# Optimization experiments

Measured on AMD Instinct MI355X. Metric: run time of the kernel, lower is better.

Reference implementation:

```python
import jax, jax.numpy as jnp
import numpy as np

N_NODES = 100000
N_EDGES = 1600000
D_IN = 64
D_HID = 64


def setup_inputs() -> dict:
    key = jax.random.key(0)
    k1, k2, k3, k4, k5 = jax.random.split(key, 5)
    x = jax.random.normal(k1, (N_NODES, D_IN), dtype=jnp.float32)
    edge_index = jax.random.randint(k2, (2, N_EDGES), 0, N_NODES, dtype=jnp.int64)
    edge_weight = jax.random.uniform(k3, (N_EDGES,), dtype=jnp.float32)
    # GCNConv glorot-initialized linear weights (bias=False)
    s0 = (6.0 / (D_IN + D_HID)) ** 0.5
    W0 = jax.random.uniform(k4, (D_IN, D_HID), minval=-s0, maxval=s0, dtype=jnp.float32)
    s1 = (6.0 / (D_HID + D_HID)) ** 0.5
    W1 = jax.random.uniform(k5, (D_HID, D_HID), minval=-s1, maxval=s1, dtype=jnp.float32)
    return {"x": x, "edge_index": edge_index, "edge_weight": edge_weight, "W0": W0, "W1": W1}


def _gcn_layer(x, W, src, dst, edge_weight, deg_inv_sqrt, n_nodes):
    # h = X W  (bias=False)
    h = x @ W  # [N, D]
    # symmetric normalization including self-loops (weight 1)
    norm = deg_inv_sqrt[src] * edge_weight * deg_inv_sqrt[dst]  # [E]
    # gather src features, scale, scatter-sum at dst
    agg = jax.ops.segment_sum(norm[:, None] * h[src], dst, num_segments=n_nodes)
    # self-loop contribution: norm_ii = deg_inv_sqrt[i]^2 * 1
    agg = agg + (deg_inv_sqrt * deg_inv_sqrt)[:, None] * h
    return jax.nn.relu(agg)  # dropout is identity in eval mode


def reference(x, edge_index, edge_weight, W0, W1):
    src, dst = edge_index[0], edge_index[1]
    # degree with self-loops (self-loop weight = 1), aggregated at dst (source_to_target flow)
    deg = jax.ops.segment_sum(edge_weight, dst, num_segments=N_NODES) + 1.0
    deg_inv_sqrt = jax.lax.rsqrt(deg)
    x = _gcn_layer(x, W0, src, dst, edge_weight, deg_inv_sqrt, N_NODES)
    x = _gcn_layer(x, W1, src, dst, edge_weight, deg_inv_sqrt, N_NODES)
    return x
```

## Files before the change

### kernel.cpp

```cpp
#include <hip/hip_runtime.h>
#include <hip/hip_fp16.h>

#define D 64
#define BSH 9
#define BSZ (1 << BSH)
#define PB 4096
#define CAPR 10240
#define CAPU (2 * CAPR)
#define FASTU (BSZ * 32)
#define SCAP 9216

__global__ __launch_bounds__(256) void initcur(int* __restrict__ ccur, int nbuck) {
    int t = threadIdx.x;
    if (t < nbuck) ccur[t] = t * CAPR;
    if (t == 255) ccur[255] = 0;
}

__global__ __launch_bounds__(512) void bucket1(const int* __restrict__ src,
                                               const int* __restrict__ dst,
                                               const float* __restrict__ ew,
                                               int* __restrict__ ccur,
                                               int2* __restrict__ pairs2,
                                               int E, int nbuck) {
    __shared__ int hist[512];
    __shared__ int lbase[512];
    __shared__ int gbase[512];
    __shared__ int w0s[PB];
    __shared__ int w1s[PB];
    __shared__ unsigned char bids[PB];
    int t = threadIdx.x;
    hist[t] = 0;
    __syncthreads();
    int e0 = blockIdx.x * PB;
    int cnt = min(PB, E - e0);
    int b[8], lr[8], w0[8], w1[8];
    int i8 = t * 8;
    bool full8 = (i8 + 8 <= cnt);
    if (full8) {
        int4   sa = *(const int4*)&src[e0 + i8];
        int4   sb = *(const int4*)&src[e0 + i8 + 4];
        int4   da = *(const int4*)&dst[e0 + i8];
        int4   db = *(const int4*)&dst[e0 + i8 + 4];
        float4 wa = *(const float4*)&ew[e0 + i8];
        float4 wb = *(const float4*)&ew[e0 + i8 + 4];
        int ss[8] = {sa.x, sa.y, sa.z, sa.w, sb.x, sb.y, sb.z, sb.w};
        int ds[8] = {da.x, da.y, da.z, da.w, db.x, db.y, db.z, db.w};
        float wv[8] = {wa.x, wa.y, wa.z, wa.w, wb.x, wb.y, wb.z, wb.w};
#pragma unroll
        for (int k = 0; k < 8; ++k) {
            b[k]  = ds[k] >> BSH;
            w0[k] = ss[k] | ((ds[k] & (BSZ - 1)) << 17);
            w1[k] = __float_as_int(wv[k]);
            lr[k] = atomicAdd(&hist[b[k]], 1);
        }
    } else {
#pragma unroll
        for (int k = 0; k < 8; ++k) {
            int idx = i8 + k;
            if (idx < cnt) {
                int d = dst[e0 + idx];
                b[k]  = d >> BSH;
                w0[k] = src[e0 + idx] | ((d & (BSZ - 1)) << 17);
                w1[k] = __float_as_int(ew[e0 + idx]);
                lr[k] = atomicAdd(&hist[b[k]], 1);
            }
        }
    }
    __syncthreads();
    int hv = hist[t];
    lbase[t] = hv;
    __syncthreads();
    for (int off = 1; off < 512; off <<= 1) {
        int u = (t >= off) ? lbase[t - off] : 0;
        __syncthreads();
        lbase[t] += u;
        __syncthreads();
    }
    int excl = lbase[t] - hv;
    __syncthreads();
    lbase[t] = excl;
    if (t < nbuck && hv > 0) gbase[t] = atomicAdd(&ccur[t], hv);
    __syncthreads();
#pragma unroll
    for (int k = 0; k < 8; ++k) {
        int idx = i8 + k;
        if (idx < cnt) {
            int slot = lbase[b[k]] + lr[k];
            w0s[slot] = w0[k];
            w1s[slot] = w1[k];
            bids[slot] = (unsigned char)b[k];
        }
    }
    __syncthreads();
    for (int i = t; i < cnt; i += 512) {
        int bb = bids[i];
        int pos = gbase[bb] + (i - lbase[bb]);
        pairs2[pos] = make_int2(w0s[i], w1s[i]);
    }
}

__global__ __launch_bounds__(512) void sort2(int2* __restrict__ pairs2,
                                             unsigned int* __restrict__ fastU,
                                             const int* __restrict__ ccur,
                                             int2* __restrict__ extRng,
                                             unsigned int* __restrict__ extU,
                                             int* __restrict__ gext,
                                             float* __restrict__ dis,
                                             int N, int nbuck) {
    __shared__ int2 se[SCAP];
    __shared__ int cnt[512];
    __shared__ float sdeg[512];
    __shared__ int ebase[512];
    int b = blockIdx.x;
    int t = threadIdx.x;
    int baseR = b * CAPR;
    int baseU = b * CAPU;
    int cntb = min(ccur[b] - baseR, SCAP);
    for (int i = t; i < cntb; i += 512) se[i] = pairs2[baseR + i];
    cnt[t] = 0;
    sdeg[t] = 0.0f;
    __syncthreads();
    for (int i = t; i < cntb; i += 512) {
        int2 p = se[i];
        int dl = (p.x >> 17) & (BSZ - 1);
        int lr = atomicAdd(&cnt[dl], 1);
        atomicAdd(&sdeg[dl], __int_as_float(p.y));
        se[i].x = p.x | (lr << 26);
    }
    __syncthreads();
    int node = (b << BSH) + t;
    int cntv = cnt[t];
    int pc = (node < N) ? ((cntv + 1 + 31) & ~31) : 0;
    int extLen = (pc > 32) ? (pc - 32) : 0;
    int extBase = 0;
    if (extLen > 0) extBase = atomicAdd(gext, extLen);
    float dloc = rsqrtf(sdeg[t] + 1.0f);
    __syncthreads();
    sdeg[t]  = dloc;
    ebase[t] = extBase;
    if (node < N) {
        extRng[node] = make_int2(extBase, extBase + extLen);
        dis[node]    = dloc;
    }
    for (int i = t; i < FASTU; i += 512) fastU[baseU + i] = 0u;
    __syncthreads();
    for (int i = t; i < cntb; i += 512) {
        int2 p = se[i];
        int dl = (p.x >> 17) & (BSZ - 1);
        int s  = p.x & 0x1FFFF;
        int rank = ((unsigned int)p.x) >> 26;
        float w = __int_as_float(p.y) * sdeg[dl];
        unsigned int h = (unsigned int)__half_as_ushort(__float2half_rn(w));
        unsigned int packed = ((unsigned int)s << 15) | ((h + 1u) >> 1);
        if (rank < 32) fastU[baseU + dl * 32 + rank] = packed;
        else           extU[ebase[dl] + rank - 32]   = packed;
    }
    if (node < N) {
        unsigned int h = (unsigned int)__half_as_ushort(__float2half_rn(dloc));
        unsigned int selfp = ((unsigned int)node << 15) | ((h + 1u) >> 1);
        if (cntv < 32) fastU[baseU + t * 32 + cntv] = selfp;
        else           extU[extBase + cntv - 32]    = selfp;
        for (int i = cntv + 1 - 32; i < extLen; ++i) extU[extBase + i] = 0u;
    }
}

__global__ __launch_bounds__(256) void gemm64h(const float* __restrict__ X,
                                               const float* __restrict__ W,
                                               const float* __restrict__ dis,
                                               __half* __restrict__ Hb, int n) {
    __shared__ float Ws[64 * 64];
    __shared__ float Xs[16 * 64];
    for (int t = threadIdx.x; t < 64 * 64; t += 256) Ws[t] = W[t];
    int row0 = blockIdx.x * 16;
    for (int t = threadIdx.x; t < 16 * 64; t += 256) {
        int r = row0 + (t >> 6);
        Xs[t] = (r < n) ? X[r * 64 + (t & 63)] : 0.0f;
    }
    __syncthreads();
    int r  = threadIdx.x >> 4;
    int jc = (threadIdx.x & 15) * 4;
    float4 acc = make_float4(0.f, 0.f, 0.f, 0.f);
#pragma unroll
    for (int k = 0; k < 64; ++k) {
        float xv = Xs[r * 64 + k];
        float4 w = *(const float4*)&Ws[k * 64 + jc];
        acc.x += xv * w.x; acc.y += xv * w.y; acc.z += xv * w.z; acc.w += xv * w.w;
    }
    int rr = row0 + r;
    if (rr < n) {
        float ds = dis[rr];
        ushort4 pk;
        pk.x = __half_as_ushort(__float2half(ds * acc.x));
        pk.y = __half_as_ushort(__float2half(ds * acc.y));
        pk.z = __half_as_ushort(__float2half(ds * acc.z));
        pk.w = __half_as_ushort(__float2half(ds * acc.w));
        *(ushort4*)&Hb[rr * 64 + jc] = pk;
    }
}

__device__ __forceinline__ void acc_group(unsigned int pv, int g, int fl,
                                          const __half* __restrict__ Hb,
                                          __half2 a0[4], __half2 a1[4],
                                          __half2 a2[4], __half2 a3[4]) {
    unsigned int q0 = __shfl(pv, g, 64);
    unsigned int q1 = __shfl(pv, g + 8, 64);
    unsigned int q2 = __shfl(pv, g + 16, 64);
    unsigned int q3 = __shfl(pv, g + 24, 64);
    uint4 r0 = *(const uint4*)(Hb + (size_t)(q0 >> 15) * 64 + fl);
    uint4 r1 = *(const uint4*)(Hb + (size_t)(q1 >> 15) * 64 + fl);
    uint4 r2 = *(const uint4*)(Hb + (size_t)(q2 >> 15) * 64 + fl);
    uint4 r3 = *(const uint4*)(Hb + (size_t)(q3 >> 15) * 64 + fl);
    __half2 w0 = __half2half2(__ushort_as_half((unsigned short)((q0 & 0x7FFFu) << 1)));
    __half2 w1 = __half2half2(__ushort_as_half((unsigned short)((q1 & 0x7FFFu) << 1)));
    __half2 w2 = __half2half2(__ushort_as_half((unsigned short)((q2 & 0x7FFFu) << 1)));
    __half2 w3 = __half2half2(__ushort_as_half((unsigned short)((q3 & 0x7FFFu) << 1)));
    const __half2* h0 = (const __half2*)&r0;
    const __half2* h1 = (const __half2*)&r1;
    const __half2* h2 = (const __half2*)&r2;
    const __half2* h3 = (const __half2*)&r3;
#pragma unroll
    for (int k = 0; k < 4; ++k) {
        a0[k] = __hfma2(w0, h0[k], a0[k]);
        a1[k] = __hfma2(w1, h1[k], a1[k]);
        a2[k] = __hfma2(w2, h2[k], a2[k]);
        a3[k] = __hfma2(w3, h3[k], a3[k]);
    }
}

__global__ __launch_bounds__(256) void gather64(const unsigned int* __restrict__ fastU,
                                                const unsigned int* __restrict__ extU,
                                                const int2* __restrict__ extRng,
                                                const __half* __restrict__ Hb,
                                                float* __restrict__ OUT, int N) {
    int node = blockIdx.x * 4 + (threadIdx.x >> 6);
    if (node >= N) return;
    int lane = threadIdx.x & 63;
    int g    = lane >> 3;
    int fl   = (lane & 7) * 8;
    int l31  = lane & 31;
    int fbase = (node >> BSH) * CAPU + (node & (BSZ - 1)) * 32;
    unsigned int pv = fastU[fbase + l31];
    int2 er = extRng[node];
    __half2 z = __float2half2_rn(0.0f);
    __half2 a0[4] = {z, z, z, z};
    __half2 a1[4] = {z, z, z, z};
    __half2 a2[4] = {z, z, z, z};
    __half2 a3[4] = {z, z, z, z};
    acc_group(pv, g, fl, Hb, a0, a1, a2, a3);
    for (int e = er.x; e < er.y; e += 32)
        acc_group(extU[e + l31], g, fl, Hb, a0, a1, a2, a3);
    __half2 a[4];
#pragma unroll
    for (int k = 0; k < 4; ++k)
        a[k] = __hadd2(__hadd2(a0[k], a1[k]), __hadd2(a2[k], a3[k]));
#pragma unroll
    for (int m = 8; m < 64; m <<= 1) {
#pragma unroll
        for (int k = 0; k < 4; ++k) {
            unsigned u = __shfl_xor(*(unsigned*)&a[k], m, 64);
            a[k] = __hadd2(a[k], *(__half2*)&u);
        }
    }
    if (g < 2) {
        int o = g * 2;
        float2 f0 = __half22float2(a[o]);
        float2 f1 = __half22float2(a[o + 1]);
        float4 vv;
        vv.x = fmaxf(f0.x, 0.0f);
        vv.y = fmaxf(f0.y, 0.0f);
        vv.z = fmaxf(f1.x, 0.0f);
        vv.w = fmaxf(f1.y, 0.0f);
        *(float4*)&OUT[node * 64 + fl + g * 4] = vv;
    }
}

extern "C" void kernel_launch(void* const* d_in, const int* in_sizes, int n_in,
                              void* d_out, int out_size, void* d_ws, size_t ws_size,
                              hipStream_t stream) {
    const float* x  = (const float*)d_in[0];
    const int*   ei = (const int*)d_in[1];
    const float* ew = (const float*)d_in[2];
    const float* W0 = (const float*)d_in[3];
    const float* W1 = (const float*)d_in[4];
    float* out = (float*)d_out;

    const int N = in_sizes[0] / D;
    const int E = in_sizes[2];
    const int* src = ei;
    const int* dst = ei + E;

    const int nbuck = (N + BSZ - 1) >> BSH;
    const int Na = (N + 1 + 255) & ~255;

    float* dis     = (float*)d_ws;
    int2*  extRng  = (int2*)((int*)d_ws + Na);
    int*   ccur    = (int*)d_ws + 3 * Na;
    int2*  pairs2  = (int2*)((int*)d_ws + 3 * Na + 1024);
    unsigned int* fastU = (unsigned int*)pairs2;
    __half* Hb     = (__half*)((int*)d_ws + 3 * Na + 1024 + (size_t)nbuck * CAPU);
    unsigned int* extU = (unsigned int*)((__half*)Hb + (size_t)N * D);

    const int nb1 = (E + PB - 1) / PB;

    initcur<<<1, 256, 0, stream>>>(ccur, nbuck);
    bucket1<<<nb1, 512, 0, stream>>>(src, dst, ew, ccur, pairs2, E, nbuck);
    sort2<<<nbuck, 512, 0, stream>>>(pairs2, fastU, ccur, extRng, extU,
                                     ccur + 255, dis, N, nbuck);

    const int gemm_grid   = (N + 15) / 16;
    const int gather_grid = (N + 3) / 4;

    gemm64h<<<gemm_grid, 256, 0, stream>>>(x, W0, dis, Hb, N);
    gather64<<<gather_grid, 256, 0, stream>>>(fastU, extU, extRng, Hb, out, N);

    gemm64h<<<gemm_grid, 256, 0, stream>>>(out, W1, dis, Hb, N);
    gather64<<<gather_grid, 256, 0, stream>>>(fastU, extU, extRng, Hb, out, N);
}
```

Before: 190.9 us.

## Use wave-shuffle scan, half-size fast slots for small nodes, fp16 intermediate layer

Result: no change. 190.2 us (-0.3%).

```diff
diff --git a/kernel.cpp b/kernel.cpp
--- a/kernel.cpp
+++ b/kernel.cpp
@@ -25,6 +25,7 @@
     __shared__ int hist[512];
     __shared__ int lbase[512];
     __shared__ int gbase[512];
+    __shared__ int wsum[8];
     __shared__ int w0s[PB];
     __shared__ int w1s[PB];
     __shared__ unsigned char bids[PB];
@@ -68,16 +69,19 @@
     }
     __syncthreads();
     int hv = hist[t];
-    lbase[t] = hv;
-    __syncthreads();
-    for (int off = 1; off < 512; off <<= 1) {
-        int u = (t >= off) ? lbase[t - off] : 0;
-        __syncthreads();
-        lbase[t] += u;
-        __syncthreads();
-    }
-    int excl = lbase[t] - hv;
-    __syncthreads();
+    int lane = t & 63, wv8 = t >> 6;
+    int s = hv;
+#pragma unroll
+    for (int off = 1; off < 64; off <<= 1) {
+        int u = __shfl_up(s, off, 64);
+        if (lane >= off) s += u;
+    }
+    if (lane == 63) wsum[wv8] = s;
+    __syncthreads();
+    int woff = 0;
+#pragma unroll
+    for (int w = 0; w < 8; ++w) { int x = wsum[w]; if (w < wv8) woff += x; }
+    int excl = s + woff - hv;
     lbase[t] = excl;
     if (t < nbuck && hv > 0) gbase[t] = atomicAdd(&ccur[t], hv);
     __syncthreads();
@@ -130,16 +134,18 @@
     __syncthreads();
     int node = (b << BSH) + t;
     int cntv = cnt[t];
-    int pc = (node < N) ? ((cntv + 1 + 31) & ~31) : 0;
+    int tot  = cntv + 1;
+    int pc   = (tot <= 16) ? 16 : ((tot + 31) & ~31);
     int extLen = (pc > 32) ? (pc - 32) : 0;
     int extBase = 0;
-    if (extLen > 0) extBase = atomicAdd(gext, extLen);
+    if (node < N && extLen > 0) extBase = atomicAdd(gext, extLen);
     float dloc = rsqrtf(sdeg[t] + 1.0f);
     __syncthreads();
     sdeg[t]  = dloc;
     ebase[t] = extBase;
     if (node < N) {
-        extRng[node] = make_int2(extBase, extBase + extLen);
+        int flag = (pc == 16) ? (1 << 30) : 0;
+        extRng[node] = make_int2(extBase | flag, extBase + extLen);
         dis[node]    = dloc;
     }
     for (int i = t; i < FASTU; i += 512) fastU[baseU + i] = 0u;
@@ -164,7 +170,8 @@
     }
 }
 
-__global__ __launch_bounds__(256) void gemm64h(const float* __restrict__ X,
+template<int HIN>
+__global__ __launch_bounds__(256) void gemm64h(const void* __restrict__ Xv,
                                                const float* __restrict__ W,
                                                const float* __restrict__ dis,
                                                __half* __restrict__ Hb, int n) {
@@ -174,7 +181,12 @@
     int row0 = blockIdx.x * 16;
     for (int t = threadIdx.x; t < 16 * 64; t += 256) {
         int r = row0 + (t >> 6);
-        Xs[t] = (r < n) ? X[r * 64 + (t & 63)] : 0.0f;
+        float v = 0.0f;
+        if (r < n) {
+            if constexpr (HIN) v = __half2float(((const __half*)Xv)[r * 64 + (t & 63)]);
+            else               v = ((const float*)Xv)[r * 64 + (t & 63)];
+        }
+        Xs[t] = v;
     }
     __syncthreads();
     int r  = threadIdx.x >> 4;
@@ -227,11 +239,12 @@
     }
 }
 
+template<int HOUT>
 __global__ __launch_bounds__(256) void gather64(const unsigned int* __restrict__ fastU,
                                                 const unsigned int* __restrict__ extU,
                                                 const int2* __restrict__ extRng,
                                                 const __half* __restrict__ Hb,
-                                                float* __restrict__ OUT, int N) {
+                                                void* __restrict__ OUTv, int N) {
     int node = blockIdx.x * 4 + (threadIdx.x >> 6);
     if (node >= N) return;
     int lane = threadIdx.x & 63;
@@ -241,13 +254,47 @@
     int fbase = (node >> BSH) * CAPU + (node & (BSZ - 1)) * 32;
     unsigned int pv = fastU[fbase + l31];
     int2 er = extRng[node];
+    bool small = (er.x & (1 << 30)) != 0;
+    int eb = er.x & 0x3FFFFFFF;
     __half2 z = __float2half2_rn(0.0f);
     __half2 a0[4] = {z, z, z, z};
     __half2 a1[4] = {z, z, z, z};
     __half2 a2[4] = {z, z, z, z};
     __half2 a3[4] = {z, z, z, z};
-    acc_group(pv, g, fl, Hb, a0, a1, a2, a3);
-    for (int e = er.x; e < er.y; e += 32)
+    {
+        unsigned int q0 = __shfl(pv, g, 64);
+        unsigned int q1 = __shfl(pv, g + 8, 64);
+        unsigned int q2 = __shfl(pv, g + 16, 64);
+        unsigned int q3 = __shfl(pv, g + 24, 64);
+        uint4 r0 = *(const uint4*)(Hb + (size_t)(q0 >> 15) * 64 + fl);
+        uint4 r1 = *(const uint4*)(Hb + (size_t)(q1 >> 15) * 64 + fl);
+        uint4 r2, r3;
+        if (!small) {
+            r2 = *(const uint4*)(Hb + (size_t)(q2 >> 15) * 64 + fl);
+            r3 = *(const uint4*)(Hb + (size_t)(q3 >> 15) * 64 + fl);
+        }
+        __half2 w0 = __half2half2(__ushort_as_half((unsigned short)((q0 & 0x7FFFu) << 1)));
+        __half2 w1 = __half2half2(__ushort_as_half((unsigned short)((q1 & 0x7FFFu) << 1)));
+        const __half2* h0 = (const __half2*)&r0;
+        const __half2* h1 = (const __half2*)&r1;
+#pragma unroll
+        for (int k = 0; k < 4; ++k) {
+            a0[k] = __hfma2(w0, h0[k], a0[k]);
+            a1[k] = __hfma2(w1, h1[k], a1[k]);
+        }
+        if (!small) {
+            __half2 w2 = __half2half2(__ushort_as_half((unsigned short)((q2 & 0x7FFFu) << 1)));
+            __half2 w3 = __half2half2(__ushort_as_half((unsigned short)((q3 & 0x7FFFu) << 1)));
+            const __half2* h2 = (const __half2*)&r2;
+            const __half2* h3 = (const __half2*)&r3;
+#pragma unroll
+            for (int k = 0; k < 4; ++k) {
+                a2[k] = __hfma2(w2, h2[k], a2[k]);
+                a3[k] = __hfma2(w3, h3[k], a3[k]);
+            }
+        }
+    }
+    for (int e = eb; e < er.y; e += 32)
         acc_group(extU[e + l31], g, fl, Hb, a0, a1, a2, a3);
     __half2 a[4];
 #pragma unroll
@@ -265,12 +312,19 @@
         int o = g * 2;
         float2 f0 = __half22float2(a[o]);
         float2 f1 = __half22float2(a[o + 1]);
-        float4 vv;
-        vv.x = fmaxf(f0.x, 0.0f);
-        vv.y = fmaxf(f0.y, 0.0f);
-        vv.z = fmaxf(f1.x, 0.0f);
-        vv.w = fmaxf(f1.y, 0.0f);
-        *(float4*)&OUT[node * 64 + fl + g * 4] = vv;
+        float rx = fmaxf(f0.x, 0.0f), ry = fmaxf(f0.y, 0.0f);
+        float rz = fmaxf(f1.x, 0.0f), rw = fmaxf(f1.y, 0.0f);
+        if constexpr (HOUT) {
+            ushort4 pk;
+            pk.x = __half_as_ushort(__float2half(rx));
+            pk.y = __half_as_ushort(__float2half(ry));
+            pk.z = __half_as_ushort(__float2half(rz));
+            pk.w = __half_as_ushort(__float2half(rw));
+            *(ushort4*)&((__half*)OUTv)[node * 64 + fl + g * 4] = pk;
+        } else {
+            float4 vv = make_float4(rx, ry, rz, rw);
+            *(float4*)&((float*)OUTv)[node * 64 + fl + g * 4] = vv;
+        }
     }
 }
 
@@ -298,7 +352,8 @@
     int2*  pairs2  = (int2*)((int*)d_ws + 3 * Na + 1024);
     unsigned int* fastU = (unsigned int*)pairs2;
     __half* Hb     = (__half*)((int*)d_ws + 3 * Na + 1024 + (size_t)nbuck * CAPU);
-    unsigned int* extU = (unsigned int*)((__half*)Hb + (size_t)N * D);
+    unsigned int* extU = (unsigned int*)(Hb + (size_t)N * D);
+    __half* x1h    = (__half*)(extU + 262144);
 
     const int nb1 = (E + PB - 1) / PB;
 
@@ -310,9 +365,9 @@
     const int gemm_grid   = (N + 15) / 16;
     const int gather_grid = (N + 3) / 4;
 
-    gemm64h<<<gemm_grid, 256, 0, stream>>>(x, W0, dis, Hb, N);
-    gather64<<<gather_grid, 256, 0, stream>>>(fastU, extU, extRng, Hb, out, N);
-
-    gemm64h<<<gemm_grid, 256, 0, stream>>>(out, W1, dis, Hb, N);
-    gather64<<<gather_grid, 256, 0, stream>>>(fastU, extU, extRng, Hb, out, N);
-}
+    gemm64h<0><<<gemm_grid, 256, 0, stream>>>(x, W0, dis, Hb, N);
+    gather64<1><<<gather_grid, 256, 0, stream>>>(fastU, extU, extRng, Hb, x1h, N);
+
+    gemm64h<1><<<gemm_grid, 256, 0, stream>>>(x1h, W1, dis, Hb, N);
+    gather64<0><<<gather_grid, 256, 0, stream>>>(fastU, extU, extRng, Hb, out, N);
+}
```
